# Performance work log

Hardware: AMD Instinct MI355X
Metric: run time of the kernel (lower is better)

Reference implementation:

```python
import jax, jax.numpy as jnp
import numpy as np

B, D_IN, D_OUT, H, E, K = 16384, 1024, 1024, 2048, 8, 2

def setup_inputs() -> dict:
    key = jax.random.key(0)
    ks = jax.random.split(key, 7)
    s_in = 1.0 / np.sqrt(D_IN)
    s_h = 1.0 / np.sqrt(H)
    return {
        "x": jax.random.normal(ks[0], (B, D_IN), dtype=jnp.float32),
        "router_W": jax.random.uniform(ks[1], (E, D_IN), jnp.float32, -s_in, s_in),
        "router_b": jax.random.uniform(ks[2], (E,), jnp.float32, -s_in, s_in),
        "W1": jax.random.uniform(ks[3], (E, H, D_IN), jnp.float32, -s_in, s_in),
        "b1": jax.random.uniform(ks[4], (E, H), jnp.float32, -s_in, s_in),
        "W2": jax.random.uniform(ks[5], (E, D_OUT, H), jnp.float32, -s_h, s_h),
        "b2": jax.random.uniform(ks[6], (E, D_OUT), jnp.float32, -s_h, s_h),
    }

def reference(x, router_W, router_b, W1, b1, W2, b2):
    # Router: softmax over experts, top-k selection, renormalize
    logits = x @ router_W.T + router_b                      # [B, E]
    router_probs = jax.nn.softmax(logits, axis=-1)          # [B, E]
    top_v, top_i = jax.lax.top_k(router_probs, K)           # [B, K]
    top_v = top_v / jnp.sum(top_v, axis=-1, keepdims=True)  # renormalized
    # Scatter top-k weights into dense [B, E] combine weights (zero elsewhere)
    b_idx = jnp.arange(x.shape[0])[:, None]
    combine = jnp.zeros_like(router_probs).at[b_idx, top_i].add(top_v)  # [B, E]
    # Dense per-expert MLP, combined with zero weights for unselected experts
    # (identical math to the original mask/gather/scatter loop)
    h = jax.nn.relu(jnp.einsum('bi,ehi->beh', x, W1) + b1)  # [B, E, H]
    y = jnp.einsum('beh,eoh->beo', h, W2) + b2              # [B, E, O]
    out = jnp.einsum('beo,be->bo', y, combine)              # [B, O]
    return out, router_probs
```

## Files before the change

kernel.cpp:

```cpp
#include <hip/hip_runtime.h>
#include <hip/hip_bf16.h>

#define Bsz  16384
#define Din  1024
#define Dout 1024
#define Hdim 2048
#define Ecnt 8
#define CNT_PAD 32

typedef _Float16 f16;
typedef _Float16 f16x8 __attribute__((ext_vector_type(8)));
typedef _Float16 f16x4 __attribute__((ext_vector_type(4)));
typedef float    f32x4 __attribute__((ext_vector_type(4)));

#define AS_GLOBAL __attribute__((address_space(1)))
#define AS_LDS    __attribute__((address_space(3)))

__device__ __forceinline__ void async_copy16(const void* gptr, void* lptr) {
    __builtin_amdgcn_global_load_lds(
        (const AS_GLOBAL unsigned int*)gptr,
        (AS_LDS unsigned int*)lptr, 16, 0, 0);
}

__global__ __launch_bounds__(256) void cast_kernel(
    const float* __restrict__ in, f16* __restrict__ out)
{
    int i = (blockIdx.x * 256 + threadIdx.x) * 4;
    float4 v = *(const float4*)(in + i);
    f16x4 o;
    o.x = (f16)v.x; o.y = (f16)v.y; o.z = (f16)v.z; o.w = (f16)v.w;
    *(f16x4*)(out + i) = o;
}

__global__ __launch_bounds__(256) void router_kernel(
    const float* __restrict__ x, const float* __restrict__ rW,
    const float* __restrict__ rb, float* __restrict__ probs_out,
    int* __restrict__ cnt, int* __restrict__ bucket, float* __restrict__ gates,
    f16* __restrict__ x16)
{
    __shared__ float s_rw[Ecnt * Din];
    __shared__ int   s_e[64];
    __shared__ float s_g[64];
    __shared__ int   s_lpos[64];
    __shared__ int   s_lcnt[Ecnt];
    __shared__ int   s_base[Ecnt];

    int t = threadIdx.x;
    if (t < Ecnt) s_lcnt[t] = 0;
    for (int i = t; i < Ecnt * Din; i += 256) s_rw[i] = rW[i];
    __syncthreads();

    int wid = t >> 6, lane = t & 63;

    float rbv[8];
    #pragma unroll
    for (int e = 0; e < 8; e++) rbv[e] = rb[e];

    #pragma unroll 2
    for (int tt = 0; tt < 8; tt++) {
        int li = wid * 8 + tt;
        int token = blockIdx.x * 32 + li;
        const float* xrow = x + (size_t)token * Din;
        f16* xorow = x16 + (size_t)token * Din;

        float acc[8] = {0,0,0,0,0,0,0,0};
        #pragma unroll
        for (int i = 0; i < 4; i++) {
            int d = i * 256 + lane * 4;
            float4 xv = *(const float4*)(xrow + d);
            f16x4 xo;
            xo.x = (f16)xv.x; xo.y = (f16)xv.y; xo.z = (f16)xv.z; xo.w = (f16)xv.w;
            *(f16x4*)(xorow + d) = xo;
            #pragma unroll
            for (int e = 0; e < 8; e++) {
                float4 wv = *(const float4*)(s_rw + e * Din + d);
                acc[e] += xv.x * wv.x + xv.y * wv.y + xv.z * wv.z + xv.w * wv.w;
            }
        }
        #pragma unroll
        for (int e = 0; e < 8; e++) {
            #pragma unroll
            for (int m = 1; m < 64; m <<= 1) acc[e] += __shfl_xor(acc[e], m, 64);
        }

        float p[8], mx = -1e30f;
        #pragma unroll
        for (int e = 0; e < 8; e++) { p[e] = acc[e] + rbv[e]; mx = fmaxf(mx, p[e]); }
        float s = 0.f;
        #pragma unroll
        for (int e = 0; e < 8; e++) { p[e] = expf(p[e] - mx); s += p[e]; }
        float inv = 1.f / s;
        #pragma unroll
        for (int e = 0; e < 8; e++) p[e] *= inv;

        if (lane == 0) {
            float* po = probs_out + (size_t)token * Ecnt;
            #pragma unroll
            for (int e = 0; e < 8; e++) po[e] = p[e];
            int i0 = 0; float v0 = p[0];
            #pragma unroll
            for (int e = 1; e < 8; e++) if (p[e] > v0) { v0 = p[e]; i0 = e; }
            int i1 = -1; float v1 = -1e30f;
            #pragma unroll
            for (int e = 0; e < 8; e++) if (e != i0 && p[e] > v1) { v1 = p[e]; i1 = e; }
            float invs = 1.f / (v0 + v1);
            s_e[2 * li]     = i0;  s_g[2 * li]     = v0 * invs;
            s_e[2 * li + 1] = i1;  s_g[2 * li + 1] = v1 * invs;
        }
    }
    __syncthreads();

    if (t < 64) s_lpos[t] = atomicAdd(&s_lcnt[s_e[t]], 1);
    __syncthreads();
    if (t < Ecnt) s_base[t] = atomicAdd(&cnt[t * CNT_PAD], s_lcnt[t]);
    __syncthreads();
    if (t < 64) {
        int e = s_e[t];
        int pos = s_base[e] + s_lpos[t];
        int li = t >> 1;
        int token = blockIdx.x * 32 + li;
        bucket[e * Bsz + pos] = token * 2 + (t & 1);
        gates [e * Bsz + pos] = s_g[t];
    }
}

template<int Kd, bool G1>
__global__ __launch_bounds__(256) void moe_gemm(
    const f16* __restrict__ A, const f16* __restrict__ Wt,
    const float* __restrict__ bias, const int* __restrict__ cnt,
    const int* __restrict__ bucket, const float* __restrict__ gates,
    f16* __restrict__ hbuf, float* __restrict__ out, int Ndim)
{
    int e   = (int)blockIdx.x & 7;
    int idx = (int)blockIdx.x >> 3;
    int nx  = Ndim >> 7;
    int by  = idx / nx;
    int bx  = idx - by * nx;

    int count = min(cnt[e * CNT_PAD], Bsz);
    int m0 = by * 128;
    if (m0 >= count) return;
    int n0 = bx * 128;

    __shared__ alignas(16) f16 As[2][128 * 32];
    __shared__ alignas(16) f16 Bs[2][128 * 32];
    __shared__ int   s_rows[128];
    __shared__ float s_gates[128];

    int t = threadIdx.x;
    if (t < 128) {
        int pos = min(m0 + t, count - 1);
        s_rows[t] = bucket[e * Bsz + pos];
        if constexpr (!G1) s_gates[t] = gates[e * Bsz + pos];
    }
    __syncthreads();

    int wave = t >> 6, lane = t & 63;
    int scol = (lane & 3) * 8;

    const f16* agp[2];
    const f16* bgp[2];
    #pragma unroll
    for (int j = 0; j < 2; j++) {
        int srow = wave * 32 + j * 16 + (lane >> 2);
        int r = s_rows[srow];
        size_t arow = G1 ? (size_t)(r >> 1) : (size_t)r;
        agp[j] = A + arow * Kd + scol;
        bgp[j] = Wt + ((size_t)e * Ndim + (n0 + srow)) * (size_t)Kd + scol;
    }

    int m_w = (wave >> 1) * 64;
    int n_w = (wave & 1) * 64;
    int frow = lane & 15;
    int fk   = (lane >> 4) * 8;

    f32x4 acc[4][4] = {};

    #pragma unroll
    for (int j = 0; j < 2; j++) {
        async_copy16(agp[j], &As[0][(wave * 32 + j * 16) * 32]);
        async_copy16(bgp[j], &Bs[0][(wave * 32 + j * 16) * 32]);
        agp[j] += 32; bgp[j] += 32;
    }
    __syncthreads();

    int cur = 0;
    for (int k0 = 0; k0 < Kd; k0 += 32) {
        if (k0 + 32 < Kd) {
            #pragma unroll
            for (int j = 0; j < 2; j++) {
                async_copy16(agp[j], &As[cur ^ 1][(wave * 32 + j * 16) * 32]);
                async_copy16(bgp[j], &Bs[cur ^ 1][(wave * 32 + j * 16) * 32]);
                agp[j] += 32; bgp[j] += 32;
            }
        }
        f16x8 af[4], bfr[4];
        #pragma unroll
        for (int i = 0; i < 4; i++) {
            af[i]  = *(const f16x8*)(&As[cur][(m_w + i * 16 + frow) * 32 + fk]);
            bfr[i] = *(const f16x8*)(&Bs[cur][(n_w + i * 16 + frow) * 32 + fk]);
        }
        __builtin_amdgcn_s_setprio(1);
        #pragma unroll
        for (int i = 0; i < 4; i++)
            #pragma unroll
            for (int jj = 0; jj < 4; jj++)
                acc[i][jj] = __builtin_amdgcn_mfma_f32_16x16x32_f16(
                    af[i], bfr[jj], acc[i][jj], 0, 0, 0);
        __builtin_amdgcn_s_setprio(0);
        __syncthreads();
        cur ^= 1;
    }

    float bv[4];
    #pragma unroll
    for (int jj = 0; jj < 4; jj++)
        bv[jj] = bias[e * Ndim + n0 + n_w + jj * 16 + frow];

    #pragma unroll
    for (int i = 0; i < 4; i++) {
        int mbase = m_w + i * 16 + (lane >> 4) * 4;
        #pragma unroll
        for (int reg = 0; reg < 4; reg++) {
            int m = mbase + reg;
            if (m0 + m >= count) continue;
            int r = s_rows[m];
            if constexpr (G1) {
                f16* hrow = hbuf + (size_t)r * Hdim;
                #pragma unroll
                for (int jj = 0; jj < 4; jj++) {
                    int n = n0 + n_w + jj * 16 + frow;
                    float v = acc[i][jj][reg] + bv[jj];
                    hrow[n] = (f16)fmaxf(v, 0.f);
                }
            } else {
                int token = r >> 1;
                float g = s_gates[m];
                #pragma unroll
                for (int jj = 0; jj < 4; jj++) {
                    int n = n0 + n_w + jj * 16 + frow;
                    float v = g * (acc[i][jj][reg] + bv[jj]);
                    atomicAdd(&out[(size_t)token * Dout + n], v);
                }
            }
        }
    }
}

extern "C" void kernel_launch(void* const* d_in, const int* in_sizes, int n_in,
                              void* d_out, int out_size, void* d_ws, size_t ws_size,
                              hipStream_t stream) {
    const float* x   = (const float*)d_in[0];
    const float* rW  = (const float*)d_in[1];
    const float* rb  = (const float*)d_in[2];
    const float* W1  = (const float*)d_in[3];
    const float* b1  = (const float*)d_in[4];
    const float* W2  = (const float*)d_in[5];
    const float* b2  = (const float*)d_in[6];
    float* out   = (float*)d_out;
    float* probs = out + (size_t)Bsz * Dout;

    char* ws = (char*)d_ws;
    int*   cnt    = (int*)ws;
    int*   bucket = (int*)(ws + 0x1000);
    float* gates  = (float*)(ws + 0x90000);
    f16*   x16    = (f16*)(ws + 0x200000);
    f16*   w16    = (f16*)(ws + 0x2200000);
    f16*   hbuf   = (f16*)(ws + 0x4200000);

    hipMemsetAsync(cnt, 0, Ecnt * CNT_PAD * sizeof(int), stream);
    hipMemsetAsync(out, 0, (size_t)Bsz * Dout * sizeof(float), stream);

    cast_kernel<<<(Ecnt * Hdim * Din) / 1024, 256, 0, stream>>>(W1, w16);

    router_kernel<<<Bsz / 32, 256, 0, stream>>>(x, rW, rb, probs, cnt, bucket, gates, x16);

    int nb1 = Ecnt * (Bsz / 128) * (Hdim / 128);
    moe_gemm<Din, true><<<nb1, 256, 0, stream>>>(
        x16, w16, b1, cnt, bucket, gates, hbuf, out, Hdim);

    cast_kernel<<<(Ecnt * Dout * Hdim) / 1024, 256, 0, stream>>>(W2, w16);

    int nb2 = Ecnt * (Bsz / 128) * (Dout / 128);
    moe_gemm<Hdim, false><<<nb2, 256, 0, stream>>>(
        hbuf, w16, b2, cnt, bucket, gates, hbuf, out, Dout);
}
```

Before: 670.3 us.

## Switch MoE GEMM to single-wave 64x64 tiles with vmcnt-based double buffering

Each MoE GEMM block shrinks from four waves on a 128x128 tile to one wave on a 64x64 tile. The k-loop is unrolled by two and issues async global-to-LDS copies into ping-pong buffers, synchronised with explicit s_waitcnt vmcnt instead of __syncthreads. The aim is to drop block-wide barriers and raise the number of resident blocks for better latency hiding. In exchange, halving the tile edge lowers data reuse, roughly doubling global/L2 traffic for A and W per flop, and multiplies the block count by four.

```diff
diff --git a/kernel.cpp b/kernel.cpp
--- a/kernel.cpp
+++ b/kernel.cpp
@@ -21,6 +21,9 @@
         (const AS_GLOBAL unsigned int*)gptr,
         (AS_LDS unsigned int*)lptr, 16, 0, 0);
 }
+
+#define WAIT_VM(n) do { asm volatile("s_waitcnt vmcnt(" #n ")" ::: "memory"); \
+                        __builtin_amdgcn_sched_barrier(0); } while (0)
 
 __global__ __launch_bounds__(256) void cast_kernel(
     const float* __restrict__ in, f16* __restrict__ out)
@@ -125,7 +128,7 @@
 }
 
 template<int Kd, bool G1>
-__global__ __launch_bounds__(256) void moe_gemm(
+__global__ __launch_bounds__(64, 3) void moe_gemm(
     const f16* __restrict__ A, const f16* __restrict__ Wt,
     const float* __restrict__ bias, const int* __restrict__ cnt,
     const int* __restrict__ bucket, const float* __restrict__ gates,
@@ -133,93 +136,95 @@
 {
     int e   = (int)blockIdx.x & 7;
     int idx = (int)blockIdx.x >> 3;
-    int nx  = Ndim >> 7;
+    int nx  = Ndim >> 6;
     int by  = idx / nx;
     int bx  = idx - by * nx;
 
     int count = min(cnt[e * CNT_PAD], Bsz);
-    int m0 = by * 128;
+    int m0 = by * 64;
     if (m0 >= count) return;
-    int n0 = bx * 128;
-
-    __shared__ alignas(16) f16 As[2][128 * 32];
-    __shared__ alignas(16) f16 Bs[2][128 * 32];
-    __shared__ int   s_rows[128];
-    __shared__ float s_gates[128];
+    int n0 = bx * 64;
+
+    __shared__ alignas(16) f16 As[2][64 * 32];
+    __shared__ alignas(16) f16 Bs[2][64 * 32];
+    __shared__ int   s_rows[64];
+    __shared__ float s_gates[64];
 
     int t = threadIdx.x;
-    if (t < 128) {
+    {
         int pos = min(m0 + t, count - 1);
         s_rows[t] = bucket[e * Bsz + pos];
         if constexpr (!G1) s_gates[t] = gates[e * Bsz + pos];
     }
     __syncthreads();
 
-    int wave = t >> 6, lane = t & 63;
-    int scol = (lane & 3) * 8;
-
-    const f16* agp[2];
-    const f16* bgp[2];
-    #pragma unroll
-    for (int j = 0; j < 2; j++) {
-        int srow = wave * 32 + j * 16 + (lane >> 2);
+    int scol = (t & 3) * 8;
+    const f16* agp[4];
+    const f16* bgp[4];
+    #pragma unroll
+    for (int j = 0; j < 4; j++) {
+        int srow = j * 16 + (t >> 2);
         int r = s_rows[srow];
         size_t arow = G1 ? (size_t)(r >> 1) : (size_t)r;
-        agp[j] = A + arow * Kd + scol;
+        agp[j] = A + arow * (size_t)Kd + scol;
         bgp[j] = Wt + ((size_t)e * Ndim + (n0 + srow)) * (size_t)Kd + scol;
     }
 
-    int m_w = (wave >> 1) * 64;
-    int n_w = (wave & 1) * 64;
-    int frow = lane & 15;
-    int fk   = (lane >> 4) * 8;
+    int frow = t & 15;
+    int fk   = (t >> 4) * 8;
 
     f32x4 acc[4][4] = {};
 
-    #pragma unroll
-    for (int j = 0; j < 2; j++) {
-        async_copy16(agp[j], &As[0][(wave * 32 + j * 16) * 32]);
-        async_copy16(bgp[j], &Bs[0][(wave * 32 + j * 16) * 32]);
-        agp[j] += 32; bgp[j] += 32;
-    }
-    __syncthreads();
-
-    int cur = 0;
-    for (int k0 = 0; k0 < Kd; k0 += 32) {
-        if (k0 + 32 < Kd) {
-            #pragma unroll
-            for (int j = 0; j < 2; j++) {
-                async_copy16(agp[j], &As[cur ^ 1][(wave * 32 + j * 16) * 32]);
-                async_copy16(bgp[j], &Bs[cur ^ 1][(wave * 32 + j * 16) * 32]);
-                agp[j] += 32; bgp[j] += 32;
-            }
-        }
-        f16x8 af[4], bfr[4];
-        #pragma unroll
-        for (int i = 0; i < 4; i++) {
-            af[i]  = *(const f16x8*)(&As[cur][(m_w + i * 16 + frow) * 32 + fk]);
-            bfr[i] = *(const f16x8*)(&Bs[cur][(n_w + i * 16 + frow) * 32 + fk]);
-        }
-        __builtin_amdgcn_s_setprio(1);
-        #pragma unroll
-        for (int i = 0; i < 4; i++)
-            #pragma unroll
-            for (int jj = 0; jj < 4; jj++)
-                acc[i][jj] = __builtin_amdgcn_mfma_f32_16x16x32_f16(
-                    af[i], bfr[jj], acc[i][jj], 0, 0, 0);
-        __builtin_amdgcn_s_setprio(0);
-        __syncthreads();
-        cur ^= 1;
-    }
+#define STAGE(buf) do { \
+        _Pragma("unroll") \
+        for (int j = 0; j < 4; j++) { \
+            async_copy16(agp[j], &As[buf][j * 512]); agp[j] += 32; } \
+        _Pragma("unroll") \
+        for (int j = 0; j < 4; j++) { \
+            async_copy16(bgp[j], &Bs[buf][j * 512]); bgp[j] += 32; } \
+    } while (0)
+
+#define COMPUTE(buf) do { \
+        f16x8 af[4], bfr[4]; \
+        _Pragma("unroll") \
+        for (int i = 0; i < 4; i++) { \
+            af[i]  = *(const f16x8*)(&As[buf][(i * 16 + frow) * 32 + fk]); \
+            bfr[i] = *(const f16x8*)(&Bs[buf][(i * 16 + frow) * 32 + fk]); } \
+        __builtin_amdgcn_s_setprio(1); \
+        _Pragma("unroll") \
+        for (int i = 0; i < 4; i++) \
+            _Pragma("unroll") \
+            for (int jj = 0; jj < 4; jj++) \
+                acc[i][jj] = __builtin_amdgcn_mfma_f32_16x16x32_f16( \
+                    af[i], bfr[jj], acc[i][jj], 0, 0, 0); \
+        __builtin_amdgcn_s_setprio(0); \
+    } while (0)
+
+    STAGE(0);
+
+    for (int k0 = 0; k0 < Kd; k0 += 64) {
+        STAGE(1);
+        WAIT_VM(8);
+        COMPUTE(0);
+        if (k0 + 64 < Kd) {
+            STAGE(0);
+            WAIT_VM(8);
+        } else {
+            WAIT_VM(0);
+        }
+        COMPUTE(1);
+    }
+#undef STAGE
+#undef COMPUTE
 
     float bv[4];
     #pragma unroll
     for (int jj = 0; jj < 4; jj++)
-        bv[jj] = bias[e * Ndim + n0 + n_w + jj * 16 + frow];
+        bv[jj] = bias[e * Ndim + n0 + jj * 16 + frow];
 
     #pragma unroll
     for (int i = 0; i < 4; i++) {
-        int mbase = m_w + i * 16 + (lane >> 4) * 4;
+        int mbase = i * 16 + (t >> 4) * 4;
         #pragma unroll
         for (int reg = 0; reg < 4; reg++) {
             int m = mbase + reg;
@@ -229,7 +234,7 @@
                 f16* hrow = hbuf + (size_t)r * Hdim;
                 #pragma unroll
                 for (int jj = 0; jj < 4; jj++) {
-                    int n = n0 + n_w + jj * 16 + frow;
+                    int n = n0 + jj * 16 + frow;
                     float v = acc[i][jj][reg] + bv[jj];
                     hrow[n] = (f16)fmaxf(v, 0.f);
                 }
@@ -238,7 +243,7 @@
                 float g = s_gates[m];
                 #pragma unroll
                 for (int jj = 0; jj < 4; jj++) {
-                    int n = n0 + n_w + jj * 16 + frow;
+                    int n = n0 + jj * 16 + frow;
                     float v = g * (acc[i][jj][reg] + bv[jj]);
                     atomicAdd(&out[(size_t)token * Dout + n], v);
                 }
@@ -275,13 +280,13 @@
 
     router_kernel<<<Bsz / 32, 256, 0, stream>>>(x, rW, rb, probs, cnt, bucket, gates, x16);
 
-    int nb1 = Ecnt * (Bsz / 128) * (Hdim / 128);
-    moe_gemm<Din, true><<<nb1, 256, 0, stream>>>(
+    int nb1 = Ecnt * (Bsz / 64) * (Hdim / 64);
+    moe_gemm<Din, true><<<nb1, 64, 0, stream>>>(
         x16, w16, b1, cnt, bucket, gates, hbuf, out, Hdim);
 
     cast_kernel<<<(Ecnt * Dout * Hdim) / 1024, 256, 0, stream>>>(W2, w16);
 
-    int nb2 = Ecnt * (Bsz / 128) * (Dout / 128);
-    moe_gemm<Hdim, false><<<nb2, 256, 0, stream>>>(
+    int nb2 = Ecnt * (Bsz / 64) * (Dout / 64);
+    moe_gemm<Hdim, false><<<nb2, 64, 0, stream>>>(
         hbuf, w16, b2, cnt, bucket, gates, hbuf, out, Dout);
 }
```

Measured after the change: 903.4 us. 1.35x slower.

## Pre-pack expert weights into MFMA fragment layout and load B directly to registers

Applied to the files above, without the earlier changes.

The weight cast kernel now writes W1/W2 in a tiled layout that matches the per-lane MFMA B-fragment order. The GEMM can then skip LDS staging for B and read fragments from global memory into registers with coalesced 16-byte loads. The main loop becomes a two-stage software pipeline with alternating register sets for B and double-buffered LDS for the gathered A rows. This cuts LDS traffic and bank pressure, but every wave fetches its B fragments straight from global or L2 memory with no sharing through LDS, and it uses more registers.

```diff
diff --git a/kernel.cpp b/kernel.cpp
--- a/kernel.cpp
+++ b/kernel.cpp
@@ -22,14 +22,28 @@
         (AS_LDS unsigned int*)lptr, 16, 0, 0);
 }
 
-__global__ __launch_bounds__(256) void cast_kernel(
-    const float* __restrict__ in, f16* __restrict__ out)
+template<int Kd, int NdimT>
+__global__ __launch_bounds__(256) void pack_kernel(
+    const float* __restrict__ in, f16* __restrict__ outp)
 {
-    int i = (blockIdx.x * 256 + threadIdx.x) * 4;
-    float4 v = *(const float4*)(in + i);
-    f16x4 o;
-    o.x = (f16)v.x; o.y = (f16)v.y; o.z = (f16)v.z; o.w = (f16)v.w;
-    *(f16x4*)(out + i) = o;
+    constexpr int KB = Kd / 32;
+    constexpr int NB = NdimT / 128;
+    int gid = blockIdx.x * 256 + threadIdx.x;
+    int l    = gid & 63;
+    int f    = (gid >> 6) & 7;
+    int kb   = (gid >> 9) % KB;
+    int rest = (gid >> 9) / KB;
+    int nb   = rest % NB;
+    int e    = rest / NB;
+    int n = nb * 128 + f * 16 + (l & 15);
+    int k = kb * 32 + (l >> 4) * 8;
+    const float* src = in + ((size_t)e * NdimT + n) * Kd + k;
+    float4 v0 = *(const float4*)(src);
+    float4 v1 = *(const float4*)(src + 4);
+    f16x8 o;
+    o[0] = (f16)v0.x; o[1] = (f16)v0.y; o[2] = (f16)v0.z; o[3] = (f16)v0.w;
+    o[4] = (f16)v1.x; o[5] = (f16)v1.y; o[6] = (f16)v1.z; o[7] = (f16)v1.w;
+    *(f16x8*)(outp + (size_t)gid * 8) = o;
 }
 
 __global__ __launch_bounds__(256) void router_kernel(
@@ -126,7 +140,7 @@
 
 template<int Kd, bool G1>
 __global__ __launch_bounds__(256) void moe_gemm(
-    const f16* __restrict__ A, const f16* __restrict__ Wt,
+    const f16* __restrict__ A, const f16* __restrict__ Wp,
     const float* __restrict__ bias, const int* __restrict__ cnt,
     const int* __restrict__ bucket, const float* __restrict__ gates,
     f16* __restrict__ hbuf, float* __restrict__ out, int Ndim)
@@ -143,7 +157,6 @@
     int n0 = bx * 128;
 
     __shared__ alignas(16) f16 As[2][128 * 32];
-    __shared__ alignas(16) f16 Bs[2][128 * 32];
     __shared__ int   s_rows[128];
     __shared__ float s_gates[128];
 
@@ -159,14 +172,12 @@
     int scol = (lane & 3) * 8;
 
     const f16* agp[2];
-    const f16* bgp[2];
     #pragma unroll
     for (int j = 0; j < 2; j++) {
         int srow = wave * 32 + j * 16 + (lane >> 2);
         int r = s_rows[srow];
         size_t arow = G1 ? (size_t)(r >> 1) : (size_t)r;
         agp[j] = A + arow * Kd + scol;
-        bgp[j] = Wt + ((size_t)e * Ndim + (n0 + srow)) * (size_t)Kd + scol;
     }
 
     int m_w = (wave >> 1) * 64;
@@ -174,43 +185,59 @@
     int frow = lane & 15;
     int fk   = (lane >> 4) * 8;
 
+    const f16* bq = Wp + (size_t)e * Ndim * Kd + (size_t)bx * (128 * Kd)
+                    + (size_t)((wave & 1) * 4) * 512 + (size_t)lane * 8;
+
     f32x4 acc[4][4] = {};
-
-    #pragma unroll
-    for (int j = 0; j < 2; j++) {
-        async_copy16(agp[j], &As[0][(wave * 32 + j * 16) * 32]);
-        async_copy16(bgp[j], &Bs[0][(wave * 32 + j * 16) * 32]);
-        agp[j] += 32; bgp[j] += 32;
-    }
-    __syncthreads();
-
-    int cur = 0;
-    for (int k0 = 0; k0 < Kd; k0 += 32) {
-        if (k0 + 32 < Kd) {
-            #pragma unroll
-            for (int j = 0; j < 2; j++) {
-                async_copy16(agp[j], &As[cur ^ 1][(wave * 32 + j * 16) * 32]);
-                async_copy16(bgp[j], &Bs[cur ^ 1][(wave * 32 + j * 16) * 32]);
-                agp[j] += 32; bgp[j] += 32;
-            }
-        }
-        f16x8 af[4], bfr[4];
-        #pragma unroll
-        for (int i = 0; i < 4; i++) {
-            af[i]  = *(const f16x8*)(&As[cur][(m_w + i * 16 + frow) * 32 + fk]);
-            bfr[i] = *(const f16x8*)(&Bs[cur][(n_w + i * 16 + frow) * 32 + fk]);
-        }
-        __builtin_amdgcn_s_setprio(1);
-        #pragma unroll
-        for (int i = 0; i < 4; i++)
-            #pragma unroll
-            for (int jj = 0; jj < 4; jj++)
-                acc[i][jj] = __builtin_amdgcn_mfma_f32_16x16x32_f16(
-                    af[i], bfr[jj], acc[i][jj], 0, 0, 0);
-        __builtin_amdgcn_s_setprio(0);
+    f16x8 bE[4], bO[4];
+
+#define STAGE_A(buf) do { \
+        _Pragma("unroll") \
+        for (int j = 0; j < 2; j++) { \
+            async_copy16(agp[j], &As[buf][(wave * 32 + j * 16) * 32]); \
+            agp[j] += 32; } \
+    } while (0)
+
+#define LOAD_B(dst) do { \
+        _Pragma("unroll") \
+        for (int jj = 0; jj < 4; jj++) dst[jj] = *(const f16x8*)(bq + jj * 512); \
+        bq += 4096; \
+    } while (0)
+
+#define COMPUTE(buf, bset) do { \
+        f16x8 af[4]; \
+        _Pragma("unroll") \
+        for (int i = 0; i < 4; i++) \
+            af[i] = *(const f16x8*)(&As[buf][(m_w + i * 16 + frow) * 32 + fk]); \
+        __builtin_amdgcn_s_setprio(1); \
+        _Pragma("unroll") \
+        for (int i = 0; i < 4; i++) \
+            _Pragma("unroll") \
+            for (int jj = 0; jj < 4; jj++) \
+                acc[i][jj] = __builtin_amdgcn_mfma_f32_16x16x32_f16( \
+                    af[i], bset[jj], acc[i][jj], 0, 0, 0); \
+        __builtin_amdgcn_s_setprio(0); \
+    } while (0)
+
+    STAGE_A(0);
+    LOAD_B(bE);
+    __syncthreads();
+
+    for (int k0 = 0; k0 < Kd; k0 += 64) {
+        STAGE_A(1);
+        LOAD_B(bO);
+        COMPUTE(0, bE);
         __syncthreads();
-        cur ^= 1;
-    }
+        if (k0 + 64 < Kd) {
+            STAGE_A(0);
+            LOAD_B(bE);
+        }
+        COMPUTE(1, bO);
+        __syncthreads();
+    }
+#undef STAGE_A
+#undef LOAD_B
+#undef COMPUTE
 
     float bv[4];
     #pragma unroll
@@ -271,7 +298,7 @@
     hipMemsetAsync(cnt, 0, Ecnt * CNT_PAD * sizeof(int), stream);
     hipMemsetAsync(out, 0, (size_t)Bsz * Dout * sizeof(float), stream);
 
-    cast_kernel<<<(Ecnt * Hdim * Din) / 1024, 256, 0, stream>>>(W1, w16);
+    pack_kernel<Din, Hdim><<<(Ecnt * Hdim * Din) / 2048, 256, 0, stream>>>(W1, w16);
 
     router_kernel<<<Bsz / 32, 256, 0, stream>>>(x, rW, rb, probs, cnt, bucket, gates, x16);
 
@@ -279,7 +306,7 @@
     moe_gemm<Din, true><<<nb1, 256, 0, stream>>>(
         x16, w16, b1, cnt, bucket, gates, hbuf, out, Hdim);
 
-    cast_kernel<<<(Ecnt * Dout * Hdim) / 1024, 256, 0, stream>>>(W2, w16);
+    pack_kernel<Hdim, Dout><<<(Ecnt * Dout * Hdim) / 2048, 256, 0, stream>>>(W2, w16);
 
     int nb2 = Ecnt * (Bsz / 128) * (Dout / 128);
     moe_gemm<Hdim, false><<<nb2, 256, 0, stream>>>(
```

Result: slower. 787.9 us (+17.6%).
